# Optimization experiments

Hardware: AMD Instinct MI355X
Metric: run time of the kernel (lower is better)

The kernel has to match this reference:

```python
import jax, jax.numpy as jnp
import numpy as np

N, E, F, H, C, G = 100000, 800000, 128, 128, 10, 128
EPS = 1e-5


def setup_inputs() -> dict:
    key = jax.random.key(0)
    ks = jax.random.split(key, 8)
    return {
        "x": jax.random.normal(ks[0], (N, F), jnp.float32),
        "edge_index": jax.random.randint(ks[1], (2, E), 0, N),
        "batch": jnp.sort(jax.random.randint(ks[2], (N,), 0, G)),
        "edge_weight": jax.random.uniform(ks[3], (E,), jnp.float32, 0.1, 1.0),
        "bn_feat_w": jnp.ones((F,), jnp.float32),
        "bn_feat_b": jnp.full((F,), 1e-4, jnp.float32),
        "conv_feat_W": jax.random.normal(ks[4], (F, H), jnp.float32) / np.float32(np.sqrt(F)),
        "conv_feat_b": jnp.zeros((H,), jnp.float32),
        "bns_w": jnp.ones((3, H), jnp.float32),
        "bns_b": jnp.full((3, H), 1e-4, jnp.float32),
        "convs_W": jax.random.normal(ks[5], (3, H, H), jnp.float32) / np.float32(np.sqrt(H)),
        "convs_b": jnp.zeros((3, H), jnp.float32),
        "bn_fc_w": jnp.ones((H,), jnp.float32),
        "bn_fc_b": jnp.full((H,), 1e-4, jnp.float32),
        "lin_fc_W": jax.random.normal(ks[6], (H, H), jnp.float32) / np.float32(np.sqrt(H)),
        "lin_fc_b": jnp.zeros((H,), jnp.float32),
        "bn_hidden_w": jnp.ones((H,), jnp.float32),
        "bn_hidden_b": jnp.full((H,), 1e-4, jnp.float32),
        "lin_class_W": jax.random.normal(ks[7], (H, C), jnp.float32) / np.float32(np.sqrt(H)),
        "lin_class_b": jnp.zeros((C,), jnp.float32),
    }


def _bn(h, w, b):
    # training-mode BatchNorm1d: biased batch stats over dim 0
    mu = h.mean(0)
    var = jnp.mean((h - mu) ** 2, 0)
    return (h - mu) * jax.lax.rsqrt(var + EPS) * w + b


def reference(x, edge_index, batch, edge_weight,
              bn_feat_w, bn_feat_b, conv_feat_W, conv_feat_b,
              bns_w, bns_b, convs_W, convs_b,
              bn_fc_w, bn_fc_b, lin_fc_W, lin_fc_b,
              bn_hidden_w, bn_hidden_b, lin_class_W, lin_class_b):
    n = x.shape[0]
    loops = jnp.arange(n)
    # PyG GCNConv: add self-loops (weight 1) + symmetric normalization, shared by all convs
    row = jnp.concatenate([edge_index[0], loops])
    col = jnp.concatenate([edge_index[1], loops])
    ew = jnp.concatenate([edge_weight, jnp.ones((n,), x.dtype)])
    deg = jax.ops.segment_sum(ew, col, num_segments=n)
    dinv = jnp.where(deg > 0, jax.lax.rsqrt(jnp.maximum(deg, EPS)), 0.0)
    norm = (dinv[row] * ew * dinv[col])[:, None]  # [E+N, 1]

    def conv(h, W, b):
        m = (h @ W)[row] * norm                 # gather + scale per edge
        return jax.ops.segment_sum(m, col, num_segments=n) + b

    h = _bn(x, bn_feat_w, bn_feat_b)
    h = jax.nn.relu(conv(h, conv_feat_W, conv_feat_b))
    h_init = h

    x_list = []
    # branch 1: BN -> Conv -> ReLU chain
    h = h_init
    for i in range(3):
        h = jax.nn.relu(conv(_bn(h, bns_w[i], bns_b[i]), convs_W[i], convs_b[i]))
    x_list.append(h)
    # branch 2: double application of the same BN/Conv per step
    h = h_init
    for i in range(3):
        h_ = jax.nn.relu(conv(_bn(h, bns_w[i], bns_b[i]), convs_W[i], convs_b[i]))
        h = jax.nn.relu(conv(_bn(h_, bns_w[i], bns_b[i]), convs_W[i], convs_b[i]))
    x_list.append(h)
    # branch 3: identical to branch 1 when conv_residual=False
    h = h_init
    for i in range(3):
        h = jax.nn.relu(conv(_bn(h, bns_w[i], bns_b[i]), convs_W[i], convs_b[i]))
    x_list.append(h)
    # branch 4: BN -> ReLU only
    h = h_init
    for i in range(3):
        h = jax.nn.relu(_bn(h, bns_w[i], bns_b[i]))
    x_list.append(h)

    def head(hn):
        g = jax.ops.segment_sum(hn, batch, num_segments=G)  # global_add_pool
        g = jax.nn.relu(_bn(g, bn_fc_w, bn_fc_b) @ lin_fc_W + lin_fc_b)
        g = _bn(g, bn_hidden_w, bn_hidden_b)
        return jax.nn.log_softmax(g @ lin_class_W + lin_class_b, axis=-1)

    return tuple(head(hn) for hn in x_list)
```

## Files before the change

kernel.cpp:

```cpp
#include <hip/hip_runtime.h>

#define N_NODES 100000
#define NPAD    100032
#define NBLK    1563
#define NEDGE   800000
#define NGRP    128
#define NSLOT   32
#define EPS     1e-5f

typedef unsigned int   u32;
typedef unsigned short u16;
typedef short bf16x8 __attribute__((ext_vector_type(8)));
typedef float f32x4  __attribute__((ext_vector_type(4)));

__device__ __forceinline__ float bf2f(u32 u){ return __uint_as_float(u << 16); }
__device__ __forceinline__ u16 f2bf(float f){
  u32 x = __float_as_uint(f);
  x += 0x7fffu + ((x >> 16) & 1u);
  return (u16)(x >> 16);
}

__global__ void k_init(float* deg, int* cnt, int* fill, float* gbuf){
  int i = blockIdx.x * 256 + threadIdx.x;
  if (i < NPAD){ deg[i] = 1.0f; cnt[i] = 0; fill[i] = 0; }
  if (i < 4 * NGRP * 128) gbuf[i] = 0.f;
}

__global__ void k_deg(const int* __restrict__ col, const float* __restrict__ ew,
                      float* __restrict__ deg, int* __restrict__ cnt){
  int e = blockIdx.x * 256 + threadIdx.x;
  if (e < NEDGE){
    int c = col[e];
    atomicAdd(&deg[c], ew[e]);
    atomicAdd(&cnt[c], 1);
  }
}

__global__ void k_dinv(const float* __restrict__ deg, float* __restrict__ dinv, float* __restrict__ srow){
  int i = blockIdx.x * 256 + threadIdx.x;
  if (i < N_NODES){
    float d = deg[i];
    float v = d > 0.f ? rsqrtf(fmaxf(d, EPS)) : 0.f;
    dinv[i] = v; srow[i] = v * v;
  }
}

__global__ __launch_bounds__(256) void k_chunksum(const int* __restrict__ cnt, int* __restrict__ csum){
  int b = blockIdx.x, t = threadIdx.x;
  int s = 0;
  for (int i = t; i < 1024; i += 256){ int idx = b * 1024 + i; if (idx < N_NODES) s += cnt[idx]; }
  __shared__ int red[256];
  red[t] = s; __syncthreads();
  for (int o = 128; o > 0; o >>= 1){ if (t < o) red[t] += red[t + o]; __syncthreads(); }
  if (t == 0) csum[b] = red[0];
}

__global__ __launch_bounds__(128) void k_chunkscan(const int* __restrict__ csum, int* __restrict__ coff,
                                                   int* __restrict__ ptrA){
  int t = threadIdx.x;
  __shared__ int s[128];
  int v = (t < 98) ? csum[t] : 0;
  s[t] = v; __syncthreads();
  for (int o = 1; o < 128; o <<= 1){
    int x = (t >= o) ? s[t - o] : 0;
    __syncthreads(); s[t] += x; __syncthreads();
  }
  if (t < 98) coff[t] = s[t] - v;
  if (t == 0) ptrA[N_NODES] = NEDGE;
}

__global__ __launch_bounds__(256) void k_scan2(const int* __restrict__ cnt, const int* __restrict__ coff,
                                               int* __restrict__ ptrA){
  int b = blockIdx.x, t = threadIdx.x;
  int base = b * 1024 + t * 4;
  int v[4], tot = 0;
  #pragma unroll
  for (int k = 0; k < 4; k++){ int idx = base + k; v[k] = (idx < N_NODES) ? cnt[idx] : 0; tot += v[k]; }
  __shared__ int sc[256];
  sc[t] = tot; __syncthreads();
  for (int o = 1; o < 256; o <<= 1){
    int x = (t >= o) ? sc[t - o] : 0;
    __syncthreads(); sc[t] += x; __syncthreads();
  }
  int off = coff[b] + sc[t] - tot;
  #pragma unroll
  for (int k = 0; k < 4; k++){ int idx = base + k; if (idx < N_NODES) ptrA[idx] = off; off += v[k]; }
}

__global__ void k_fill(const int* __restrict__ row, const int* __restrict__ col,
                       const float* __restrict__ ew, const float* __restrict__ dinv,
                       const int* __restrict__ ptrA, int* __restrict__ fill, int2* __restrict__ adj,
                       float* __restrict__ srow){
  int e = blockIdx.x * 256 + threadIdx.x;
  if (e < NEDGE){
    int r = row[e], c = col[e];
    float w = dinv[r] * ew[e] * dinv[c];
    int pos = ptrA[c] + atomicAdd(&fill[c], 1);
    adj[pos] = make_int2(r, __float_as_int(w));
    atomicAdd(&srow[c], w);
  }
}

__global__ __launch_bounds__(256) void k_bhist(const int* __restrict__ batch, int* __restrict__ bpart){
  __shared__ int loc[128];
  int t = threadIdx.x;
  if (t < 128) loc[t] = 0;
  __syncthreads();
  int i = blockIdx.x * 256 + t;
  if (i < N_NODES) atomicAdd(&loc[batch[i]], 1);
  __syncthreads();
  if (t < 128) bpart[blockIdx.x * 128 + t] = loc[t];
}

__global__ __launch_bounds__(128) void k_bscan(const int* __restrict__ bpart, int* __restrict__ gptr){
  int t = threadIdx.x;
  int v = 0;
  for (int p = 0; p < 391; p++) v += bpart[p * 128 + t];
  __shared__ int s[128];
  s[t] = v; __syncthreads();
  for (int o = 1; o < 128; o <<= 1){
    int x = (t >= o) ? s[t - o] : 0;
    __syncthreads(); s[t] += x; __syncthreads();
  }
  gptr[t + 1] = s[t];
  if (t == 0) gptr[0] = 0;
}

__global__ __launch_bounds__(256) void k_cvtstats(const float* __restrict__ x, u32* __restrict__ dst,
                                                  float* __restrict__ sums_out){
  __shared__ float R[1024];
  int t = threadIdx.x;
  float s0 = 0.f, q0 = 0.f, s1 = 0.f, q1 = 0.f;
  size_t base = (size_t)blockIdx.x * 4096 + t;
  #pragma unroll
  for (int it = 0; it < 16; it++){
    size_t idx = base + (size_t)it * 256;
    if (idx < (size_t)N_NODES * 64){
      float2 v = ((const float2*)x)[idx];
      dst[idx] = (u32)f2bf(v.x) | ((u32)f2bf(v.y) << 16);
      s0 += v.x; q0 += v.x * v.x; s1 += v.y; q1 += v.y * v.y;
    }
  }
  R[t] = s0; R[256 + t] = q0; R[512 + t] = s1; R[768 + t] = q1;
  __syncthreads();
  if (t < 64){
    float S0 = 0.f, Q0 = 0.f, S1 = 0.f, Q1 = 0.f;
    #pragma unroll
    for (int g = 0; g < 4; g++){
      S0 += R[g * 64 + t];       Q0 += R[256 + g * 64 + t];
      S1 += R[512 + g * 64 + t]; Q1 += R[768 + g * 64 + t];
    }
    float* so = sums_out + (blockIdx.x & (NSLOT - 1)) * 256;
    atomicAdd(&so[2 * t], S0);
    atomicAdd(&so[2 * t + 1], S1);
    atomicAdd(&so[128 + 2 * t], Q0);
    atomicAdd(&so[128 + 2 * t + 1], Q1);
  }
}

__device__ __forceinline__ void fold_body(int blk, int t, const float* __restrict__ sums,
    const float* __restrict__ bw, const float* __restrict__ bb,
    const float* __restrict__ W, const float* __restrict__ bias,
    u16* __restrict__ Wh, u16* __restrict__ Wl, float* __restrict__ rb,
    float* scl, float* shf, float* stot, float* rred){
  {
    float s = 0.f;
    #pragma unroll 4
    for (int sl = 0; sl < NSLOT; sl++) s += sums[sl * 256 + t];
    stot[t] = s;
  }
  __syncthreads();
  if (t < 128){
    float mu  = stot[t] * (1.f / N_NODES);
    float var = stot[128 + t] * (1.f / N_NODES) - mu * mu;
    float sc  = bw[t] * rsqrtf(var + EPS);
    scl[t] = sc; shf[t] = bb[t] - mu * sc;
  }
  __syncthreads();
  {
    int idx = blk * 256 + t;
    int lane_ = idx & 63, sl = idx >> 6;
    int nt_ = sl >> 2, ks_ = sl & 3;
    int n_ = nt_ * 16 + (lane_ & 15);
    int kb = ks_ * 32 + (lane_ >> 4) * 8;
    u16 hi8[8], lo8[8];
    #pragma unroll
    for (int j = 0; j < 8; j++){
      float wv = W[(kb + j) * 128 + n_];
      float xv = scl[kb + j] * wv;
      u16 hh = f2bf(xv);
      hi8[j] = hh; lo8[j] = f2bf(xv - bf2f(hh));
    }
    uint4 ph, pl;
    ph.x = (u32)hi8[0] | ((u32)hi8[1] << 16); ph.y = (u32)hi8[2] | ((u32)hi8[3] << 16);
    ph.z = (u32)hi8[4] | ((u32)hi8[5] << 16); ph.w = (u32)hi8[6] | ((u32)hi8[7] << 16);
    pl.x = (u32)lo8[0] | ((u32)lo8[1] << 16); pl.y = (u32)lo8[2] | ((u32)lo8[3] << 16);
    pl.z = (u32)lo8[4] | ((u32)lo8[5] << 16); pl.w = (u32)lo8[6] | ((u32)lo8[7] << 16);
    *(uint4*)&Wh[idx * 8] = ph;
    *(uint4*)&Wl[idx * 8] = pl;
  }
  {
    int nl = t & 15, kk = t >> 4;
    int n2 = blk * 16 + nl;
    float rp = 0.f;
    #pragma unroll
    for (int j = 0; j < 8; j++){
      int k2 = kk * 8 + j;
      rp += shf[k2] * W[k2 * 128 + n2];
    }
    rred[t] = rp;
  }
  __syncthreads();
  if (t < 16){
    float s = 0.f;
    #pragma unroll
    for (int kk2 = 0; kk2 < 16; kk2++) s += rred[kk2 * 16 + t];
    int n2 = blk * 16 + t;
    rb[n2] = s;
    rb[128 + n2] = bias[n2];
  }
}

__global__ __launch_bounds__(256) void k_fold(const float* __restrict__ sums,
    const float* __restrict__ bw, const float* __restrict__ bb,
    const float* __restrict__ W, const float* __restrict__ bias,
    u16* __restrict__ Wh, u16* __restrict__ Wl, float* __restrict__ rb){
  __shared__ float scl[128], shf[128], stot[256], rred[256];
  fold_body(blockIdx.x, threadIdx.x, sums, bw, bb, W, bias, Wh, Wl, rb, scl, shf, stot, rred);
}

__global__ __launch_bounds__(256) void k_fold2(
    const float* __restrict__ sumsA, const float* __restrict__ bwA, const float* __restrict__ bbA,
    const float* __restrict__ WA, const float* __restrict__ biasA,
    u16* __restrict__ WhA, u16* __restrict__ WlA, float* __restrict__ rbA,
    const float* __restrict__ sumsB, const float* __restrict__ bwB, const float* __restrict__ bbB,
    const float* __restrict__ WB, const float* __restrict__ biasB,
    u16* __restrict__ WhB, u16* __restrict__ WlB, float* __restrict__ rbB){
  __shared__ float scl[128], shf[128], stot[256], rred[256];
  int bb_ = blockIdx.x;
  if (bb_ < 8)
    fold_body(bb_, threadIdx.x, sumsA, bwA, bbA, WA, biasA, WhA, WlA, rbA, scl, shf, stot, rred);
  else
    fold_body(bb_ - 8, threadIdx.x, sumsB, bwB, bbB, WB, biasB, WhB, WlB, rbB, scl, shf, stot, rred);
}

#define CONV_EPILOGUE(RB, HOUT, SOUT, BLK)                                     \
  __syncthreads();                                                             \
  sred[t] = 0.f;                                                               \
  __syncthreads();                                                             \
  _Pragma("unroll")                                                            \
  for (int nt = 0; nt < 8; nt++){                                              \
    int colc = nt * 16 + m;                                                    \
    float rv = RB[colc], bv = RB[128 + colc];                                  \
    float s = 0.f, qq = 0.f;                                                   \
    _Pragma("unroll")                                                          \
    for (int r = 0; r < 4; r++){                                               \
      int rown = row0 + q * 4 + r;                                             \
      float v = C[nt][r] + srow[rown] * rv + bv;                               \
      v = fmaxf(v, 0.f);                                                       \
      u16 sv = f2bf(v);                                                        \
      HOUT[(size_t)rown * 128 + colc] = sv;                                    \
      if (rown < N_NODES){ float vv = bf2f(sv); s += vv; qq += vv * vv; }      \
    }                                                                          \
    s  += __shfl_xor(s, 16, 64);  s  += __shfl_xor(s, 32, 64);                 \
    qq += __shfl_xor(qq, 16, 64); qq += __shfl_xor(qq, 32, 64);                \
    if (q == 0){                                                               \
      atomicAdd(&sred[colc], s);                                               \
      atomicAdd(&sred[128 + colc], qq);                                        \
    }                                                                          \
  }                                                                            \
  __syncthreads();                                                             \
  atomicAdd(&SOUT[((BLK) & (NSLOT - 1)) * 256 + t], sred[t]);

#define FMA_KS(KS, V, WT) \
  acc[KS][0] += (WT) * __uint_as_float((V).x << 16); acc[KS][1] += (WT) * __uint_as_float((V).x & 0xffff0000u); \
  acc[KS][2] += (WT) * __uint_as_float((V).y << 16); acc[KS][3] += (WT) * __uint_as_float((V).y & 0xffff0000u); \
  acc[KS][4] += (WT) * __uint_as_float((V).z << 16); acc[KS][5] += (WT) * __uint_as_float((V).z & 0xffff0000u); \
  acc[KS][6] += (WT) * __uint_as_float((V).w << 16); acc[KS][7] += (WT) * __uint_as_float((V).w & 0xffff0000u);

__device__ __forceinline__ void gather_row(const u16* __restrict__ h,
    const int* __restrict__ ptrA, const int2* __restrict__ adj,
    const float* __restrict__ dinv, int i, int q, float (&acc)[4][8]){
  #pragma unroll
  for (int ks = 0; ks < 4; ks++)
    #pragma unroll
    for (int j = 0; j < 8; j++) acc[ks][j] = 0.f;
  if (i >= N_NODES) return;
  const u16* hq = h + q * 8;
  float di = dinv[i], sw = di * di;
  uint4 s0 = *(const uint4*)(hq + (size_t)i * 128);
  uint4 s1 = *(const uint4*)(hq + (size_t)i * 128 + 32);
  uint4 s2 = *(const uint4*)(hq + (size_t)i * 128 + 64);
  uint4 s3 = *(const uint4*)(hq + (size_t)i * 128 + 96);
  int b = ptrA[i], e = ptrA[i + 1];
  int k = b;
  int2 a0 = make_int2(0, 0), a1 = a0, a2 = a0, a3 = a0;
  if (k + 4 <= e){ a0 = adj[k]; a1 = adj[k + 1]; a2 = adj[k + 2]; a3 = adj[k + 3]; }
  __builtin_amdgcn_sched_barrier(0);
  FMA_KS(0, s0, sw) FMA_KS(1, s1, sw) FMA_KS(2, s2, sw) FMA_KS(3, s3, sw)
  while (k + 4 <= e){
    const u16* p0 = hq + (size_t)a0.x * 128;
    const u16* p1 = hq + (size_t)a1.x * 128;
    const u16* p2 = hq + (size_t)a2.x * 128;
    const u16* p3 = hq + (size_t)a3.x * 128;
    uint4 u0 = *(const uint4*)(p0);      uint4 u1 = *(const uint4*)(p0 + 32);
    uint4 u2 = *(const uint4*)(p0 + 64); uint4 u3 = *(const uint4*)(p0 + 96);
    uint4 v0 = *(const uint4*)(p1);      uint4 v1 = *(const uint4*)(p1 + 32);
    uint4 v2 = *(const uint4*)(p1 + 64); uint4 v3 = *(const uint4*)(p1 + 96);
    uint4 w0 = *(const uint4*)(p2);      uint4 w1 = *(const uint4*)(p2 + 32);
    uint4 w2 = *(const uint4*)(p2 + 64); uint4 w3 = *(const uint4*)(p2 + 96);
    uint4 y0 = *(const uint4*)(p3);      uint4 y1 = *(const uint4*)(p3 + 32);
    uint4 y2 = *(const uint4*)(p3 + 64); uint4 y3 = *(const uint4*)(p3 + 96);
    float f0 = __int_as_float(a0.y), f1 = __int_as_float(a1.y);
    float f2 = __int_as_float(a2.y), f3 = __int_as_float(a3.y);
    k += 4;
    if (k + 4 <= e){ a0 = adj[k]; a1 = adj[k + 1]; a2 = adj[k + 2]; a3 = adj[k + 3]; }
    __builtin_amdgcn_sched_barrier(0);
    FMA_KS(0, u0, f0) FMA_KS(1, u1, f0) FMA_KS(2, u2, f0) FMA_KS(3, u3, f0)
    FMA_KS(0, v0, f1) FMA_KS(1, v1, f1) FMA_KS(2, v2, f1) FMA_KS(3, v3, f1)
    FMA_KS(0, w0, f2) FMA_KS(1, w1, f2) FMA_KS(2, w2, f2) FMA_KS(3, w3, f2)
    FMA_KS(0, y0, f3) FMA_KS(1, y1, f3) FMA_KS(2, y2, f3) FMA_KS(3, y3, f3)
  }
  if (k + 2 <= e){
    int2 a0t = adj[k], a1t = adj[k + 1];
    const u16* r0p = hq + (size_t)a0t.x * 128;
    const u16* r1p = hq + (size_t)a1t.x * 128;
    uint4 u0 = *(const uint4*)(r0p);      uint4 u1 = *(const uint4*)(r0p + 32);
    uint4 u2 = *(const uint4*)(r0p + 64); uint4 u3 = *(const uint4*)(r0p + 96);
    uint4 w0 = *(const uint4*)(r1p);      uint4 w1 = *(const uint4*)(r1p + 32);
    uint4 w2 = *(const uint4*)(r1p + 64); uint4 w3 = *(const uint4*)(r1p + 96);
    float f0 = __int_as_float(a0t.y), f1 = __int_as_float(a1t.y);
    FMA_KS(0, u0, f0) FMA_KS(1, u1, f0) FMA_KS(2, u2, f0) FMA_KS(3, u3, f0)
    FMA_KS(0, w0, f1) FMA_KS(1, w1, f1) FMA_KS(2, w2, f1) FMA_KS(3, w3, f1)
    k += 2;
  }
  if (k < e){
    int2 a0t = adj[k];
    const u16* r0p = hq + (size_t)a0t.x * 128;
    uint4 u0 = *(const uint4*)(r0p);      uint4 u1 = *(const uint4*)(r0p + 32);
    uint4 u2 = *(const uint4*)(r0p + 64); uint4 u3 = *(const uint4*)(r0p + 96);
    float f0 = __int_as_float(a0t.y);
    FMA_KS(0, u0, f0) FMA_KS(1, u1, f0) FMA_KS(2, u2, f0) FMA_KS(3, u3, f0)
  }
}

#define BUILD_AFRAG()                                                          \
  bf16x8 AH[4], AL[4];                                                         \
  _Pragma("unroll")                                                            \
  for (int ks = 0; ks < 4; ks++)                                               \
    _Pragma("unroll")                                                          \
    for (int j = 0; j < 8; j++){                                               \
      u16 hh = f2bf(acc[ks][j]);                                               \
      AH[ks][j] = (short)hh;                                                   \
      AL[ks][j] = (short)f2bf(acc[ks][j] - bf2f(hh));                          \
    }

#define MFMA_3PASS(WH, WL_)                                                    \
  _Pragma("unroll")                                                            \
  for (int ks = 0; ks < 4; ks++){                                              \
    _Pragma("unroll")                                                          \
    for (int nt = 0; nt < 8; nt++){                                            \
      bf16x8 bh = ((const bf16x8*)WH)[(nt * 4 + ks) * 64 + lane];              \
      bf16x8 bl = ((const bf16x8*)WL_)[(nt * 4 + ks) * 64 + lane];             \
      C[nt] = __builtin_amdgcn_mfma_f32_16x16x32_bf16(AH[ks], bh, C[nt], 0, 0, 0); \
      C[nt] = __builtin_amdgcn_mfma_f32_16x16x32_bf16(AL[ks], bh, C[nt], 0, 0, 0); \
      C[nt] = __builtin_amdgcn_mfma_f32_16x16x32_bf16(AH[ks], bl, C[nt], 0, 0, 0); \
    }                                                                          \
  }

__global__ __launch_bounds__(256, 3) void k_conv(
    const u16* __restrict__ h, const int* __restrict__ ptrA, const int2* __restrict__ adj,
    const float* __restrict__ dinv, const float* __restrict__ srow,
    const u16* __restrict__ Wh, const u16* __restrict__ Wl, const float* __restrict__ rb,
    u16* __restrict__ hout, float* __restrict__ sums_out){
  __shared__ float sred[256];
  int t = threadIdx.x;
  int wave = t >> 6, lane = t & 63, m = lane & 15, q = lane >> 4;
  int blk = blockIdx.x;
  int row0 = blk * 64 + wave * 16;
  int i = row0 + m;
  float acc[4][8];
  gather_row(h, ptrA, adj, dinv, i, q, acc);
  BUILD_AFRAG()
  f32x4 C[8];
  #pragma unroll
  for (int nt = 0; nt < 8; nt++) C[nt] = f32x4{0.f, 0.f, 0.f, 0.f};
  MFMA_3PASS(Wh, Wl)
  CONV_EPILOGUE(rb, hout, sums_out, blk)
}

__global__ __launch_bounds__(256, 3) void k_conv2(
    const u16* __restrict__ hA, const u16* __restrict__ hB,
    const int* __restrict__ ptrA, const int2* __restrict__ adj,
    const float* __restrict__ dinv, const float* __restrict__ srow,
    const u16* __restrict__ WhA, const u16* __restrict__ WlA, const float* __restrict__ rbA,
    u16* __restrict__ houtA, float* __restrict__ sumsA,
    const u16* __restrict__ WhB, const u16* __restrict__ WlB, const float* __restrict__ rbB,
    u16* __restrict__ houtB, float* __restrict__ sumsB){
  __shared__ float sred[256];
  int t = threadIdx.x;
  int wave = t >> 6, lane = t & 63, m = lane & 15, q = lane >> 4;
  int bb = blockIdx.x;
  int second = bb >= NBLK;
  int blk = second ? bb - NBLK : bb;
  const u16* h = second ? hB : hA;
  const u16* Wh = second ? WhB : WhA;
  const u16* Wl = second ? WlB : WlA;
  const float* rb = second ? rbB : rbA;
  u16* hout = second ? houtB : houtA;
  float* sums_out = second ? sumsB : sumsA;
  int row0 = blk * 64 + wave * 16;
  int i = row0 + m;
  float acc[4][8];
  gather_row(h, ptrA, adj, dinv, i, q, acc);
  BUILD_AFRAG()
  f32x4 C[8];
  #pragma unroll
  for (int nt = 0; nt < 8; nt++) C[nt] = f32x4{0.f, 0.f, 0.f, 0.f};
  MFMA_3PASS(Wh, Wl)
  CONV_EPILOGUE(rb, hout, sums_out, blk)
}

__global__ __launch_bounds__(256, 3) void k_dualconv(
    const u16* __restrict__ h, const int* __restrict__ ptrA, const int2* __restrict__ adj,
    const float* __restrict__ dinv, const float* __restrict__ srow,
    const u16* __restrict__ Wh1, const u16* __restrict__ Wl1, const float* __restrict__ rb1,
    u16* __restrict__ hout1, float* __restrict__ sums1,
    const u16* __restrict__ Wh2, const u16* __restrict__ Wl2, const float* __restrict__ rb2,
    u16* __restrict__ hout2, float* __restrict__ sums2){
  __shared__ float sred[256];
  int t = threadIdx.x;
  int wave = t >> 6, lane = t & 63, m = lane & 15, q = lane >> 4;
  int blk = blockIdx.x;
  int row0 = blk * 64 + wave * 16;
  int i = row0 + m;
  float acc[4][8];
  gather_row(h, ptrA, adj, dinv, i, q, acc);
  BUILD_AFRAG()
  f32x4 C[8];
  #pragma unroll
  for (int nt = 0; nt < 8; nt++) C[nt] = f32x4{0.f, 0.f, 0.f, 0.f};
  MFMA_3PASS(Wh1, Wl1)
  CONV_EPILOGUE(rb1, hout1, sums1, blk)
  #pragma unroll
  for (int nt = 0; nt < 8; nt++) C[nt] = f32x4{0.f, 0.f, 0.f, 0.f};
  MFMA_3PASS(Wh2, Wl2)
  CONV_EPILOGUE(rb2, hout2, sums2, blk)
}

__global__ __launch_bounds__(256) void k_normrelu(const u16* __restrict__ h, const float* __restrict__ sums,
    const float* __restrict__ bw, const float* __restrict__ bb, u16* __restrict__ o,
    float* __restrict__ sums_out){
  __shared__ float scl[128], shf[128], R[1024], stot[256];
  int t = threadIdx.x;
  {
    float s = 0.f;
    #pragma unroll 4
    for (int sl = 0; sl < NSLOT; sl++) s += sums[sl * 256 + t];
    stot[t] = s;
  }
  __syncthreads();
  if (t < 128){
    float mu  = stot[t] * (1.f / N_NODES);
    float var = stot[128 + t] * (1.f / N_NODES) - mu * mu;
    float sc  = bw[t] * rsqrtf(var + EPS);
    scl[t] = sc; shf[t] = bb[t] - mu * sc;
  }
  __syncthreads();
  int c0 = (t & 63) * 2;
  float sc0 = scl[c0], sh0 = shf[c0], sc1 = scl[c0 + 1], sh1 = shf[c0 + 1];
  float s0 = 0.f, q0 = 0.f, s1 = 0.f, q1 = 0.f;
  size_t base = (size_t)blockIdx.x * 4096 + t;
  #pragma unroll
  for (int it = 0; it < 16; it++){
    size_t idx = base + (size_t)it * 256;
    if (idx < (size_t)N_NODES * 64){
      u32 v = ((const u32*)h)[idx];
      float x0 = fmaxf(bf2f(v & 0xffffu) * sc0 + sh0, 0.f);
      float x1 = fmaxf(bf2f(v >> 16) * sc1 + sh1, 0.f);
      u16 r0 = f2bf(x0), r1 = f2bf(x1);
      ((u32*)o)[idx] = (u32)r0 | ((u32)r1 << 16);
      float y0 = bf2f(r0), y1 = bf2f(r1);
      s0 += y0; q0 += y0 * y0; s1 += y1; q1 += y1 * y1;
    }
  }
  R[t] = s0; R[256 + t] = q0; R[512 + t] = s1; R[768 + t] = q1;
  __syncthreads();
  if (t < 64){
    float S0 = 0.f, Q0 = 0.f, S1 = 0.f, Q1 = 0.f;
    #pragma unroll
    for (int g = 0; g < 4; g++){
      S0 += R[g * 64 + t];       Q0 += R[256 + g * 64 + t];
      S1 += R[512 + g * 64 + t]; Q1 += R[768 + g * 64 + t];
    }
    float* so = sums_out + (blockIdx.x & (NSLOT - 1)) * 256;
    atomicAdd(&so[2 * t], S0);
    atomicAdd(&so[2 * t + 1], S1);
    atomicAdd(&so[128 + 2 * t], Q0);
    atomicAdd(&so[128 + 2 * t + 1], Q1);
  }
}

__global__ __launch_bounds__(128) void k_pool(const u16* __restrict__ h, const int* __restrict__ gptr,
                                              float* __restrict__ gdst){
  int g = blockIdx.x >> 3, s = blockIdx.x & 7, t = threadIdx.x;
  int b = gptr[g], e = gptr[g + 1];
  int len = e - b, per = (len + 7) >> 3;
  int r0 = b + s * per, r1 = min(r0 + per, e);
  float acc = 0.f;
  for (int r = r0; r < r1; r++) acc += bf2f(h[(size_t)r * 128 + t]);
  atomicAdd(&gdst[g * 128 + t], acc);
}

__global__ __launch_bounds__(256) void k_head(const float* __restrict__ gbuf,
    const float* __restrict__ fcw, const float* __restrict__ fcb,
    const float* __restrict__ Wfc, const float* __restrict__ bfc,
    const float* __restrict__ bhw, const float* __restrict__ bhb,
    const float* __restrict__ Wcl, const float* __restrict__ bcl,
    float* __restrict__ out){
  __shared__ float GS[128 * 65];
  __shared__ float ls[256], lq[256];
  __shared__ float scl[128], shf[128], scl2[128], shf2[128];
  __shared__ float sumT[128], sumQ[128];
  __shared__ float WclT[1280], Lrow[1280];
  int t = threadIdx.x, br = blockIdx.x;
  int slot = (br == 1) ? 1 : (br == 3 ? 3 : 0);
  const float* G = gbuf + slot * 16384;
  {
    int col = t & 127, hf2 = t >> 7;
    float s = 0.f, q = 0.f;
    for (int g = hf2 * 64; g < hf2 * 64 + 64; g++){ float v = G[g * 128 + col]; s += v; q += v * v; }
    ls[t] = s; lq[t] = q;
  }
  for (int idx = t; idx < 1280; idx += 256){
    int cc = idx >> 7, c = idx & 127;
    WclT[idx] = Wcl[c * 10 + cc];
  }
  if (t < 128){ sumT[t] = 0.f; sumQ[t] = 0.f; }
  __syncthreads();
  if (t < 128){
    float s = ls[t] + ls[t + 128], q = lq[t] + lq[t + 128];
    float mu = s * (1.f / 128), var = q * (1.f / 128) - mu * mu;
    float sc = fcw[t] * rsqrtf(var + EPS);
    scl[t] = sc; shf[t] = fcb[t] - mu * sc;
  }
  __syncthreads();
  int tr = t >> 4, tc = t & 15, r0 = tr * 8, c0 = tc * 8;
  float acc[8][8];
  #pragma unroll
  for (int a = 0; a < 8; a++)
    #pragma unroll
    for (int b = 0; b < 8; b++) acc[a][b] = 0.f;
  for (int kh = 0; kh < 2; kh++){
    for (int idx = t; idx < 8192; idx += 256){
      int r = idx >> 6, kk = idx & 63, f = kh * 64 + kk;
      GS[r * 65 + kk] = G[r * 128 + f] * scl[f] + shf[f];
    }
    __syncthreads();
    #pragma unroll 2
    for (int k = 0; k < 64; k++){
      float a[8];
      #pragma unroll
      for (int ri = 0; ri < 8; ri++) a[ri] = GS[(r0 + ri) * 65 + k];
      float4 b0 = *(const float4*)&Wfc[(kh * 64 + k) * 128 + c0];
      float4 b1 = *(const float4*)&Wfc[(kh * 64 + k) * 128 + c0 + 4];
      float bb[8] = {b0.x, b0.y, b0.z, b0.w, b1.x, b1.y, b1.z, b1.w};
      #pragma unroll
      for (int ri = 0; ri < 8; ri++)
        #pragma unroll
        for (int ci = 0; ci < 8; ci++) acc[ri][ci] += a[ri] * bb[ci];
    }
    __syncthreads();
  }
  #pragma unroll
  for (int ci = 0; ci < 8; ci++){
    float bb = bfc[c0 + ci];
    float s = 0.f, q = 0.f;
    #pragma unroll
    for (int ri = 0; ri < 8; ri++){
      float v = fmaxf(acc[ri][ci] + bb, 0.f);
      acc[ri][ci] = v; s += v; q += v * v;
    }
    atomicAdd(&sumT[c0 + ci], s);
    atomicAdd(&sumQ[c0 + ci], q);
  }
  __syncthreads();
  if (t < 128){
    float mu = sumT[t] * (1.f / 128), var = sumQ[t] * (1.f / 128) - mu * mu;
    float sc = bhw[t] * rsqrtf(var + EPS);
    scl2[t] = sc; shf2[t] = bhb[t] - mu * sc;
  }
  __syncthreads();
  #pragma unroll
  for (int ci = 0; ci < 8; ci++){
    float sc = scl2[c0 + ci], sh = shf2[c0 + ci];
    #pragma unroll
    for (int ri = 0; ri < 8; ri++) acc[ri][ci] = acc[ri][ci] * sc + sh;
  }
  #pragma unroll
  for (int ri = 0; ri < 8; ri++){
    float pl[10];
    #pragma unroll
    for (int cc = 0; cc < 10; cc++) pl[cc] = 0.f;
    #pragma unroll
    for (int ci = 0; ci < 8; ci++){
      float v = acc[ri][ci];
      #pragma unroll
      for (int cc = 0; cc < 10; cc++) pl[cc] += v * WclT[cc * 128 + c0 + ci];
    }
    #pragma unroll
    for (int msk = 1; msk < 16; msk <<= 1)
      #pragma unroll
      for (int cc = 0; cc < 10; cc++) pl[cc] += __shfl_xor(pl[cc], msk, 64);
    if (tc == 0)
      #pragma unroll
      for (int cc = 0; cc < 10; cc++) Lrow[(r0 + ri) * 10 + cc] = pl[cc];
  }
  __syncthreads();
  if (t < 128){
    float l[10];
    #pragma unroll
    for (int cc = 0; cc < 10; cc++) l[cc] = Lrow[t * 10 + cc] + bcl[cc];
    float m = l[0];
    #pragma unroll
    for (int cc = 1; cc < 10; cc++) m = fmaxf(m, l[cc]);
    float se = 0.f;
    #pragma unroll
    for (int cc = 0; cc < 10; cc++) se += expf(l[cc] - m);
    float lse = m + logf(se);
    #pragma unroll
    for (int cc = 0; cc < 10; cc++) out[br * 1280 + t * 10 + cc] = l[cc] - lse;
  }
}

extern "C" void kernel_launch(void* const* d_in, const int* in_sizes, int n_in,
                              void* d_out, int out_size, void* d_ws, size_t ws_size,
                              hipStream_t stream){
  const float* x    = (const float*)d_in[0];
  const int*  ei    = (const int*)d_in[1];
  const int*  batch = (const int*)d_in[2];
  const float* ew   = (const float*)d_in[3];
  const float* bnfw = (const float*)d_in[4];
  const float* bnfb = (const float*)d_in[5];
  const float* cfW  = (const float*)d_in[6];
  const float* cfb  = (const float*)d_in[7];
  const float* bnsw = (const float*)d_in[8];
  const float* bnsb = (const float*)d_in[9];
  const float* cvW  = (const float*)d_in[10];
  const float* cvb  = (const float*)d_in[11];
  const float* fcw  = (const float*)d_in[12];
  const float* fcb  = (const float*)d_in[13];
  const float* Wfc  = (const float*)d_in[14];
  const float* bfc  = (const float*)d_in[15];
  const float* bhw  = (const float*)d_in[16];
  const float* bhb  = (const float*)d_in[17];
  const float* Wcl  = (const float*)d_in[18];
  const float* bcl  = (const float*)d_in[19];
  float* out = (float*)d_out;

  char* p = (char*)d_ws;
  auto carve = [&](size_t bytes)->void*{ void* r = (void*)p; p += (bytes + 255) & ~(size_t)255; return r; };
  float* deg  = (float*)carve((size_t)NPAD * 4);
  float* dinv = (float*)carve((size_t)NPAD * 4);
  float* srow = (float*)carve((size_t)NPAD * 4);
  int*   cnt  = (int*)carve((size_t)NPAD * 4);
  int*   fill = (int*)carve((size_t)NPAD * 4);
  int*   ptrA = (int*)carve((size_t)(NPAD + 1) * 4);
  int*   bpart= (int*)carve((size_t)391 * 128 * 4);
  int*   csum = (int*)carve(512);
  int*   coff = (int*)carve(512);
  int*   gptr = (int*)carve(1024);
  float* S    = (float*)carve((size_t)13 * NSLOT * 1024);
  float* gbuf = (float*)carve(4 * 128 * 128 * 4);
  u16*   F0h  = (u16*)carve(32768);  u16* F0l = (u16*)carve(32768);  float* F0r = (float*)carve(1024);
  u16*   F1h  = (u16*)carve(32768);  u16* F1l = (u16*)carve(32768);  float* F1r = (float*)carve(1024);
  u16*   F2h  = (u16*)carve(32768);  u16* F2l = (u16*)carve(32768);  float* F2r = (float*)carve(1024);
  u16*   B0   = (u16*)carve((size_t)NPAD * 256);
  u16*   B1   = (u16*)carve((size_t)NPAD * 256);
  u16*   B2   = (u16*)carve((size_t)NPAD * 256);
  u16*   B3   = (u16*)carve((size_t)NPAD * 256);
  int2*  adj  = (int2*)carve((size_t)NEDGE * 8);
  u16*   Xb   = B3;
  auto Sb = [&](int i){ return S + (size_t)i * NSLOT * 256; };

  (void)hipMemsetAsync(S, 0, (size_t)13 * NSLOT * 1024, stream);

  k_init<<<392, 256, 0, stream>>>(deg, cnt, fill, gbuf);
  k_deg<<<3125, 256, 0, stream>>>(ei + NEDGE, ew, deg, cnt);
  k_dinv<<<391, 256, 0, stream>>>(deg, dinv, srow);
  k_chunksum<<<98, 256, 0, stream>>>(cnt, csum);
  k_chunkscan<<<1, 128, 0, stream>>>(csum, coff, ptrA);
  k_scan2<<<98, 256, 0, stream>>>(cnt, coff, ptrA);
  k_fill<<<3125, 256, 0, stream>>>(ei, ei + NEDGE, ew, dinv, ptrA, fill, adj, srow);
  k_bhist<<<391, 256, 0, stream>>>(batch, bpart);
  k_bscan<<<1, 128, 0, stream>>>(bpart, gptr);
  k_cvtstats<<<NBLK, 256, 0, stream>>>(x, (u32*)Xb, Sb(0));

  auto fold = [&](const float* Sin, const float* bw, const float* bb,
                  const float* W, const float* bias, u16* Fh, u16* Fl, float* Fr){
    k_fold<<<8, 256, 0, stream>>>(Sin, bw, bb, W, bias, Fh, Fl, Fr);
  };
  auto conv = [&](const u16* hin, const u16* Fh, const u16* Fl, const float* Fr,
                  u16* hout, float* Sout){
    k_conv<<<NBLK, 256, 0, stream>>>(hin, ptrA, adj, dinv, srow, Fh, Fl, Fr, hout, Sout);
  };

  fold(Sb(0), bnfw, bnfb, cfW, cfb, F0h, F0l, F0r);
  conv(Xb, F0h, F0l, F0r, B0, Sb(1));
  fold(Sb(1), bnsw, bnsb, cvW, cvb, F1h, F1l, F1r);
  conv(B0, F1h, F1l, F1r, B1, Sb(2));
  k_normrelu<<<NBLK, 256, 0, stream>>>(B0, Sb(1), bnsw,       bnsb,       B2, Sb(3));
  k_normrelu<<<NBLK, 256, 0, stream>>>(B2, Sb(3), bnsw + 128, bnsb + 128, B3, Sb(4));
  k_normrelu<<<NBLK, 256, 0, stream>>>(B3, Sb(4), bnsw + 256, bnsb + 256, B2, Sb(12));
  k_pool<<<1024, 128, 0, stream>>>(B2, gptr, gbuf + 3 * 16384);
  k_fold2<<<16, 256, 0, stream>>>(
      Sb(2), bnsw + 128, bnsb + 128, cvW + 16384, cvb + 128, F0h, F0l, F0r,
      Sb(2), bnsw,       bnsb,       cvW,         cvb,       F1h, F1l, F1r);
  k_dualconv<<<NBLK, 256, 0, stream>>>(B1, ptrA, adj, dinv, srow,
      F0h, F0l, F0r, B3, Sb(5),
      F1h, F1l, F1r, B2, Sb(6));
  k_fold2<<<16, 256, 0, stream>>>(
      Sb(5), bnsw + 256, bnsb + 256, cvW + 32768, cvb + 256, F2h, F2l, F2r,
      Sb(6), bnsw + 128, bnsb + 128, cvW + 16384, cvb + 128, F0h, F0l, F0r);
  k_conv2<<<2 * NBLK, 256, 0, stream>>>(B3, B2, ptrA, adj, dinv, srow,
      F2h, F2l, F2r, B0, Sb(10),
      F0h, F0l, F0r, B1, Sb(7));
  k_pool<<<1024, 128, 0, stream>>>(B0, gptr, gbuf);
  fold(Sb(7), bnsw + 128, bnsb + 128, cvW + 16384, cvb + 128, F1h, F1l, F1r);
  conv(B1, F1h, F1l, F1r, B2, Sb(8));
  fold(Sb(8), bnsw + 256, bnsb + 256, cvW + 32768, cvb + 256, F2h, F2l, F2r);
  conv(B2, F2h, F2l, F2r, B1, Sb(9));
  fold(Sb(9), bnsw + 256, bnsb + 256, cvW + 32768, cvb + 256, F0h, F0l, F0r);
  conv(B1, F0h, F0l, F0r, B3, Sb(11));
  k_pool<<<1024, 128, 0, stream>>>(B3, gptr, gbuf + 16384);

  k_head<<<4, 256, 0, stream>>>(gbuf, fcw, fcb, Wfc, bfc, bhw, bhb, Wcl, bcl, out);
}
```

Before: 1.088 ms.

## Stage neighbor-row gathers through LDS with async global_load_lds double buffering

Replaces the register-based 4-way unrolled neighbor gather with a per-wave double-buffered LDS staging pipeline. It issues global_load_lds copies with an XOR swizzle and uses explicit vmcnt waits, so loads for the next edge overlap FMAs on the current one. Each wave loops to the maximum degree among its 16 rows, which adds divergence waste on high-degree rows. It also adds 32KB of LDS per block, which may lower occupancy under the 3-blocks launch bound.

```diff
diff --git a/kernel.cpp b/kernel.cpp
--- a/kernel.cpp
+++ b/kernel.cpp
@@ -278,69 +278,87 @@
   acc[KS][4] += (WT) * __uint_as_float((V).z << 16); acc[KS][5] += (WT) * __uint_as_float((V).z & 0xffff0000u); \
   acc[KS][6] += (WT) * __uint_as_float((V).w << 16); acc[KS][7] += (WT) * __uint_as_float((V).w & 0xffff0000u);
 
-__device__ __forceinline__ void gather_row(const u16* __restrict__ h,
+#define VMCNT6() asm volatile("s_waitcnt vmcnt(6)" ::: "memory")
+#define VMCNT5() asm volatile("s_waitcnt vmcnt(5)" ::: "memory")
+#define SB0()    __builtin_amdgcn_sched_barrier(0)
+
+
+__device__ __forceinline__ void gll_stage(const u16* __restrict__ h, u16* dst, int2 aj, int lane){
+  int c = lane & 15, g = lane >> 4;
+  #pragma unroll
+  for (int ii = 0; ii < 4; ii++){
+    int rl = ii * 4 + g;
+    int srcrow = __shfl(aj.x, rl, 64);
+    const u16* src = h + (size_t)srcrow * 128 + (size_t)((c ^ rl) * 8);
+    __builtin_amdgcn_global_load_lds((const void*)src, (void*)(dst + ii * 512), 16, 0, 0);
+  }
+}
+
+#define GITER(WA, WB, WC, WD, STG, J)                                          \
+  WD = *(const int2*)(adj + base_ + min((J) + 3, dcl));                        \
+  VMCNT6();                                                                    \
+  {                                                                            \
+    float wgt = __int_as_float(__shfl((WA).y, m, 64));                         \
+    if ((J) < deg){                                                            \
+      const u16* sp = stage + (STG) * 2048;                                    \
+      _Pragma("unroll")                                                        \
+      for (int ks = 0; ks < 4; ks++){                                          \
+        int slot = (q + 4 * ks) ^ m;                                           \
+        uint4 v = *(const uint4*)(sp + m * 128 + slot * 8);                    \
+        FMA_KS(ks, v, wgt)                                                     \
+      }                                                                        \
+    }                                                                          \
+  }                                                                            \
+  VMCNT5();                                                                    \
+  gll_stage(h, stage + (STG) * 2048, WC, lane);                                \
+  SB0();
+
+__device__ __forceinline__ void gather_row_lds(const u16* __restrict__ h,
     const int* __restrict__ ptrA, const int2* __restrict__ adj,
-    const float* __restrict__ dinv, int i, int q, float (&acc)[4][8]){
+    const float* __restrict__ dinv, int row0, int lane, u16* stage,
+    float (&acc)[4][8]){
+  int m = lane & 15, q = lane >> 4;
   #pragma unroll
   for (int ks = 0; ks < 4; ks++)
     #pragma unroll
     for (int j = 0; j < 8; j++) acc[ks][j] = 0.f;
-  if (i >= N_NODES) return;
+  int r = row0 + m;
+  int r2 = min(r, N_NODES - 1);
+  int b0 = ptrA[r2], b1 = ptrA[r2 + 1];
+  int deg = (r < N_NODES) ? (b1 - b0) : 0;
+  int base_ = b0;
+  int dcl = max(deg - 1, 0);
+  float di = dinv[r2];
+  float sw = (r < N_NODES) ? di * di : 0.f;
   const u16* hq = h + q * 8;
-  float di = dinv[i], sw = di * di;
-  uint4 s0 = *(const uint4*)(hq + (size_t)i * 128);
-  uint4 s1 = *(const uint4*)(hq + (size_t)i * 128 + 32);
-  uint4 s2 = *(const uint4*)(hq + (size_t)i * 128 + 64);
-  uint4 s3 = *(const uint4*)(hq + (size_t)i * 128 + 96);
-  int b = ptrA[i], e = ptrA[i + 1];
-  int k = b;
-  int2 a0 = make_int2(0, 0), a1 = a0, a2 = a0, a3 = a0;
-  if (k + 4 <= e){ a0 = adj[k]; a1 = adj[k + 1]; a2 = adj[k + 2]; a3 = adj[k + 3]; }
-  __builtin_amdgcn_sched_barrier(0);
+  const u16* sp_ = hq + (size_t)r2 * 128;
+  uint4 s0 = *(const uint4*)(sp_);
+  uint4 s1 = *(const uint4*)(sp_ + 32);
+  uint4 s2 = *(const uint4*)(sp_ + 64);
+  uint4 s3 = *(const uint4*)(sp_ + 96);
+  int2 W0 = *(const int2*)(adj + base_);
+  int2 W1 = *(const int2*)(adj + base_ + min(1, dcl));
+  int wmax = deg;
+  wmax = max(wmax, __shfl_xor(wmax, 1, 64));
+  wmax = max(wmax, __shfl_xor(wmax, 2, 64));
+  wmax = max(wmax, __shfl_xor(wmax, 4, 64));
+  wmax = max(wmax, __shfl_xor(wmax, 8, 64));
   FMA_KS(0, s0, sw) FMA_KS(1, s1, sw) FMA_KS(2, s2, sw) FMA_KS(3, s3, sw)
-  while (k + 4 <= e){
-    const u16* p0 = hq + (size_t)a0.x * 128;
-    const u16* p1 = hq + (size_t)a1.x * 128;
-    const u16* p2 = hq + (size_t)a2.x * 128;
-    const u16* p3 = hq + (size_t)a3.x * 128;
-    uint4 u0 = *(const uint4*)(p0);      uint4 u1 = *(const uint4*)(p0 + 32);
-    uint4 u2 = *(const uint4*)(p0 + 64); uint4 u3 = *(const uint4*)(p0 + 96);
-    uint4 v0 = *(const uint4*)(p1);      uint4 v1 = *(const uint4*)(p1 + 32);
-    uint4 v2 = *(const uint4*)(p1 + 64); uint4 v3 = *(const uint4*)(p1 + 96);
-    uint4 w0 = *(const uint4*)(p2);      uint4 w1 = *(const uint4*)(p2 + 32);
-    uint4 w2 = *(const uint4*)(p2 + 64); uint4 w3 = *(const uint4*)(p2 + 96);
-    uint4 y0 = *(const uint4*)(p3);      uint4 y1 = *(const uint4*)(p3 + 32);
-    uint4 y2 = *(const uint4*)(p3 + 64); uint4 y3 = *(const uint4*)(p3 + 96);
-    float f0 = __int_as_float(a0.y), f1 = __int_as_float(a1.y);
-    float f2 = __int_as_float(a2.y), f3 = __int_as_float(a3.y);
-    k += 4;
-    if (k + 4 <= e){ a0 = adj[k]; a1 = adj[k + 1]; a2 = adj[k + 2]; a3 = adj[k + 3]; }
-    __builtin_amdgcn_sched_barrier(0);
-    FMA_KS(0, u0, f0) FMA_KS(1, u1, f0) FMA_KS(2, u2, f0) FMA_KS(3, u3, f0)
-    FMA_KS(0, v0, f1) FMA_KS(1, v1, f1) FMA_KS(2, v2, f1) FMA_KS(3, v3, f1)
-    FMA_KS(0, w0, f2) FMA_KS(1, w1, f2) FMA_KS(2, w2, f2) FMA_KS(3, w3, f2)
-    FMA_KS(0, y0, f3) FMA_KS(1, y1, f3) FMA_KS(2, y2, f3) FMA_KS(3, y3, f3)
-  }
-  if (k + 2 <= e){
-    int2 a0t = adj[k], a1t = adj[k + 1];
-    const u16* r0p = hq + (size_t)a0t.x * 128;
-    const u16* r1p = hq + (size_t)a1t.x * 128;
-    uint4 u0 = *(const uint4*)(r0p);      uint4 u1 = *(const uint4*)(r0p + 32);
-    uint4 u2 = *(const uint4*)(r0p + 64); uint4 u3 = *(const uint4*)(r0p + 96);
-    uint4 w0 = *(const uint4*)(r1p);      uint4 w1 = *(const uint4*)(r1p + 32);
-    uint4 w2 = *(const uint4*)(r1p + 64); uint4 w3 = *(const uint4*)(r1p + 96);
-    float f0 = __int_as_float(a0t.y), f1 = __int_as_float(a1t.y);
-    FMA_KS(0, u0, f0) FMA_KS(1, u1, f0) FMA_KS(2, u2, f0) FMA_KS(3, u3, f0)
-    FMA_KS(0, w0, f1) FMA_KS(1, w1, f1) FMA_KS(2, w2, f1) FMA_KS(3, w3, f1)
-    k += 2;
-  }
-  if (k < e){
-    int2 a0t = adj[k];
-    const u16* r0p = hq + (size_t)a0t.x * 128;
-    uint4 u0 = *(const uint4*)(r0p);      uint4 u1 = *(const uint4*)(r0p + 32);
-    uint4 u2 = *(const uint4*)(r0p + 64); uint4 u3 = *(const uint4*)(r0p + 96);
-    float f0 = __int_as_float(a0t.y);
-    FMA_KS(0, u0, f0) FMA_KS(1, u1, f0) FMA_KS(2, u2, f0) FMA_KS(3, u3, f0)
+  if (wmax > 0){
+    int2 W2 = W0, W3 = W0;
+    SB0();
+    gll_stage(h, stage, W0, lane);
+    SB0();
+    W2 = *(const int2*)(adj + base_ + min(2, dcl));
+    SB0();
+    gll_stage(h, stage + 2048, W1, lane);
+    SB0();
+    for (int j0 = 0; j0 < wmax; j0 += 4){
+      GITER(W0, W1, W2, W3, 0, j0)
+      GITER(W1, W2, W3, W0, 1, j0 + 1)
+      GITER(W2, W3, W0, W1, 0, j0 + 2)
+      GITER(W3, W0, W1, W2, 1, j0 + 3)
+    }
   }
 }
 
@@ -373,14 +391,14 @@
     const float* __restrict__ dinv, const float* __restrict__ srow,
     const u16* __restrict__ Wh, const u16* __restrict__ Wl, const float* __restrict__ rb,
     u16* __restrict__ hout, float* __restrict__ sums_out){
+  __shared__ u16 hstage[4][2][2048];
   __shared__ float sred[256];
   int t = threadIdx.x;
   int wave = t >> 6, lane = t & 63, m = lane & 15, q = lane >> 4;
   int blk = blockIdx.x;
   int row0 = blk * 64 + wave * 16;
-  int i = row0 + m;
   float acc[4][8];
-  gather_row(h, ptrA, adj, dinv, i, q, acc);
+  gather_row_lds(h, ptrA, adj, dinv, row0, lane, &hstage[wave][0][0], acc);
   BUILD_AFRAG()
   f32x4 C[8];
   #pragma unroll
@@ -397,6 +415,7 @@
     u16* __restrict__ houtA, float* __restrict__ sumsA,
     const u16* __restrict__ WhB, const u16* __restrict__ WlB, const float* __restrict__ rbB,
     u16* __restrict__ houtB, float* __restrict__ sumsB){
+  __shared__ u16 hstage[4][2][2048];
   __shared__ float sred[256];
   int t = threadIdx.x;
   int wave = t >> 6, lane = t & 63, m = lane & 15, q = lane >> 4;
@@ -410,9 +429,8 @@
   u16* hout = second ? houtB : houtA;
   float* sums_out = second ? sumsB : sumsA;
   int row0 = blk * 64 + wave * 16;
-  int i = row0 + m;
   float acc[4][8];
-  gather_row(h, ptrA, adj, dinv, i, q, acc);
+  gather_row_lds(h, ptrA, adj, dinv, row0, lane, &hstage[wave][0][0], acc);
   BUILD_AFRAG()
   f32x4 C[8];
   #pragma unroll
@@ -428,14 +446,14 @@
     u16* __restrict__ hout1, float* __restrict__ sums1,
     const u16* __restrict__ Wh2, const u16* __restrict__ Wl2, const float* __restrict__ rb2,
     u16* __restrict__ hout2, float* __restrict__ sums2){
+  __shared__ u16 hstage[4][2][2048];
   __shared__ float sred[256];
   int t = threadIdx.x;
   int wave = t >> 6, lane = t & 63, m = lane & 15, q = lane >> 4;
   int blk = blockIdx.x;
   int row0 = blk * 64 + wave * 16;
-  int i = row0 + m;
   float acc[4][8];
-  gather_row(h, ptrA, adj, dinv, i, q, acc);
+  gather_row_lds(h, ptrA, adj, dinv, row0, lane, &hstage[wave][0][0], acc);
   BUILD_AFRAG()
   f32x4 C[8];
   #pragma unroll
```

Result: no change. 1.094 ms (+0.6%).
